# Kernel tuning notes

Measured on AMD Instinct MI355X. Metric: run time of the kernel, lower is better.

The kernel has to match this reference:

```python
import jax, jax.numpy as jnp
import numpy as np

V, E, H = 50000, 128, 256  # vocab, embedding_size, hidden_size
S, B = 512, 64             # seq_len, batch (seq-first, torch LSTM default)


def setup_inputs() -> dict:
    key = jax.random.key(0)
    ks = jax.random.split(key, 10)
    u = 1.0 / np.sqrt(H)  # torch LSTM/Linear init bound

    def unif(k, sh):
        return jax.random.uniform(k, sh, jnp.float32, -u, u)

    emb = jax.random.normal(ks[0], (V, E), jnp.float32) * 0.02
    emb = emb.at[0].set(0.0)  # padding_idx=0

    inp = {
        "seq": jax.random.randint(ks[1], (S, B), 0, V),
        "emb": emb,
        # forward direction weights (gate order i,f,g,o like torch)
        "W_ih_f": unif(ks[2], (4 * H, E)),
        "W_hh_f": unif(ks[3], (4 * H, H)),
        "b_f": unif(ks[4], (4 * H,)),  # b_ih + b_hh fused (identical math)
        # reverse direction
        "W_ih_b": unif(ks[5], (4 * H, E)),
        "W_hh_b": unif(ks[6], (4 * H, H)),
        "b_b": unif(ks[7], (4 * H,)),
        # classification head over concatenated bi-directional features
        "W_out": unif(ks[8], (1, 2 * H)),
        "b_out": unif(ks[9], (1,)),
    }
    return inp


def _lstm_scan(xg, W_hh):
    """xg: [S,B,4H] precomputed input-gate projections; returns hidden seq [S,B,H]."""
    b = xg.shape[1]
    h0 = jnp.zeros((b, H), xg.dtype)
    c0 = jnp.zeros((b, H), xg.dtype)

    def step(carry, xg_t):
        h, c = carry
        gates = xg_t + h @ W_hh.T  # [B,4H]
        i, f, g, o = jnp.split(gates, 4, axis=-1)
        i = jax.nn.sigmoid(i)
        f = jax.nn.sigmoid(f)
        g = jnp.tanh(g)
        o = jax.nn.sigmoid(o)
        c = f * c + i * g
        h = o * jnp.tanh(c)
        return (h, c), h

    _, hs = jax.lax.scan(step, (h0, c0), xg)
    return hs


def reference(seq, emb, W_ih_f, W_hh_f, b_f, W_ih_b, W_hh_b, b_b, W_out, b_out):
    # embedding with padding_idx=0 (row 0 contributes zero)
    x = jnp.where((seq == 0)[..., None], 0.0, emb[seq])  # [S,B,E]

    xg_f = jnp.einsum("sbe,ge->sbg", x, W_ih_f) + b_f          # [S,B,4H]
    hs_f = _lstm_scan(xg_f, W_hh_f)                             # [S,B,H]

    xr = x[::-1]
    xg_b = jnp.einsum("sbe,ge->sbg", xr, W_ih_b) + b_b
    hs_b = _lstm_scan(xg_b, W_hh_b)[::-1]                       # [S,B,H]

    out = jnp.concatenate([hs_f, hs_b], axis=-1)                # [S,B,2H]
    last = out[-1]                                              # [B,2H]
    return jax.nn.sigmoid(last @ W_out.T + b_out)               # [B,1]
```

## Files before the change

### kernel.cpp

```cpp
#include <hip/hip_runtime.h>
#include <hip/hip_bf16.h>
#include <stdint.h>
#include <string.h>

#define S_LEN 512
#define NBATCH 64
#define EDIM 128
#define HDIM 256
#define GDIM 1024

#define WQ_SCALE 1024.0f
#define HQ_SCALE 127.0f
#define LOG2E 1.4426950408889634f
#define C_IFO (-1.1093545e-05f)
#define C_G (2.2187090e-05f)

typedef __attribute__((ext_vector_type(8))) short short8;
typedef __attribute__((ext_vector_type(4))) short short4v;
typedef __attribute__((ext_vector_type(4))) float float4v;
typedef __attribute__((ext_vector_type(4))) int int4v;

#define OFF_WHH8 0u
#define SZ_WHH8 (256u * 64u * 16u)
#define OFF_WIH (OFF_WHH8 + SZ_WHH8)
#define SZ_WIH (64u * 4u * 64u * 16u)
#define OFF_XG ((size_t)(OFF_WIH + SZ_WIH))
#define SZ_XG ((size_t)S_LEN * NBATCH * GDIM * 2)
#define OFF_HF (OFF_XG + SZ_XG)

__device__ __forceinline__ short f2bf(float f) {
    union { float f; unsigned u; } v;
    v.f = f;
    unsigned r = (v.u + 0x7fffu + ((v.u >> 16) & 1u)) >> 16;
    return (short)r;
}
__device__ __forceinline__ float bf2f(short s) {
    union { unsigned u; float f; } v;
    v.u = ((unsigned)(unsigned short)s) << 16;
    return v.f;
}
__device__ __forceinline__ float sigm(float x) {
    float e = __expf(-x);
    return __builtin_amdgcn_rcpf(1.0f + e);
}
__device__ __forceinline__ float tanh_(float x) {
    float e = __expf(2.0f * x);
    return 1.0f - 2.0f * __builtin_amdgcn_rcpf(e + 1.0f);
}

__global__ __launch_bounds__(256) void prep_frags(const float* __restrict__ src,
                                                  char* __restrict__ dst,
                                                  int K, int nchunks, int nfrags) {
    int id = blockIdx.x * blockDim.x + threadIdx.x;
    int lane = id & 63;
    int f = id >> 6;
    if (f >= nfrags) return;
    int tile = f / nchunks;
    int c = f - tile * nchunks;
    int row = tile * 16 + (lane & 15);
    int k0 = c * 32 + ((lane >> 4) * 8);
    const float* s = src + (size_t)row * K + k0;
    short8 pack;
#pragma unroll
    for (int j = 0; j < 8; ++j) pack[j] = f2bf(s[j]);
    *(short8*)(dst + ((size_t)f * 64 + lane) * 16) = pack;
}

__global__ __launch_bounds__(256) void prep_whh_i8(const float* __restrict__ src,
                                                   char* __restrict__ dst) {
    int id = blockIdx.x * blockDim.x + threadIdx.x;
    int lane = id & 63;
    int f = id >> 6;
    int tile = f >> 2, kc = f & 3;
    int row = tile * 16 + (lane & 15);
    int k0 = kc * 64 + ((lane >> 4) * 16);
    const float* s = src + (size_t)row * HDIM + k0;
    union { char b[16]; int4v v; } u;
#pragma unroll
    for (int b = 0; b < 16; ++b)
        u.b[b] = (char)(int)rintf(s[b] * WQ_SCALE);
    *(int4v*)(dst + ((size_t)f * 64 + lane) * 16) = u.v;
}

__global__ __launch_bounds__(256) void input_proj(const int* __restrict__ seq,
                                                  const float* __restrict__ emb,
                                                  const char* __restrict__ wih_frags,
                                                  const float* __restrict__ bias,
                                                  char* __restrict__ xg) {
    __shared__ __align__(16) short lx[4][16][136];
    int tid = threadIdx.x;
    int t0 = blockIdx.x * 4;
    int g = blockIdx.y;

    {
        int row = tid >> 2;
        int tt = row >> 4, m = row & 15;
        int k0 = (tid & 3) * 32;
        int v = seq[(t0 + tt) * NBATCH + g * 16 + m];
        const float* src = emb + (size_t)v * EDIM + k0;
        bool zero = (v == 0);
#pragma unroll
        for (int u = 0; u < 32; u += 4) {
            float4v f = *(const float4v*)(src + u);
            short4v p;
#pragma unroll
            for (int e = 0; e < 4; ++e) p[e] = zero ? (short)0 : f2bf(f[e]);
            *(short4v*)&lx[tt][m][k0 + u] = p;
        }
    }
    __syncthreads();

    int lane = tid & 63, w = tid >> 6;
    int ln = lane & 15, q = lane >> 4;

    short8 Bx[4][4];
#pragma unroll
    for (int tt = 0; tt < 4; ++tt)
#pragma unroll
        for (int c = 0; c < 4; ++c)
            Bx[tt][c] = *(const short8*)&lx[tt][ln][c * 32 + q * 8];

    for (int nt = 0; nt < 16; ++nt) {
        int tile = w * 16 + nt;
        float kg = ((tile >> 4) == 2) ? (2.0f * LOG2E) : (-LOG2E);
        short8 Aw[4];
#pragma unroll
        for (int c = 0; c < 4; ++c)
            Aw[c] = *(const short8*)(wih_frags + (((size_t)tile * 4 + c) * 64 + lane) * 16);
        float4v b4 = *(const float4v*)(bias + tile * 16 + q * 4);
#pragma unroll
        for (int tt = 0; tt < 4; ++tt) {
            float4v acc = b4;
#pragma unroll
            for (int c = 0; c < 4; ++c)
                acc = __builtin_amdgcn_mfma_f32_16x16x32_bf16(Aw[c], Bx[tt][c], acc, 0, 0, 0);
            short4v p;
#pragma unroll
            for (int r = 0; r < 4; ++r) p[r] = f2bf(acc[r] * kg);
            size_t off = ((size_t)(t0 + tt) * NBATCH + g * 16 + ln) * GDIM + tile * 16 + q * 4;
            *(short4v*)(xg + off * 2) = p;
        }
    }
}

#define HPAD 320
__global__ __launch_bounds__(1024, 4) void lstm_scan(const char* __restrict__ whh8,
                                                     const char* __restrict__ xg,
                                                     float* __restrict__ hf_out) {
    __shared__ __align__(16) char hls[2][4][HPAD];
    __shared__ __align__(16) int scr[16][256];
    int tid = threadIdx.x;
    int lane = tid & 63, w = tid >> 6;
    int ln = lane & 15, q = lane >> 4;
    int bg = blockIdx.x;

    int4v Wfr[4][4];
#pragma unroll
    for (int g = 0; g < 4; ++g) {
        int tile = g * 16 + w;
#pragma unroll
        for (int kc = 0; kc < 4; ++kc)
            Wfr[g][kc] = *(const int4v*)(whh8 + (((size_t)(tile * 4 + kc)) * 64 + lane) * 16);
    }

    {
        int* hp = (int*)&hls[0][0][0];
        for (int i = tid; i < (2 * 4 * HPAD) / 4; i += 1024) hp[i] = 0;
    }

    const char* hrd = &hls[0][0][0];
    char* hwr = &hls[1][0][0];
    int hoff_rd = (ln & 3) * HPAD + q * 16;

    int b = ln & 3;
    int rr = ln >> 2;
    int j = w * 16 + q * 4 + rr;
    int hoff_wr = b * HPAD + j;

    int* swr = &scr[w][q * 16 + ln * 4];
    const int* srd = &scr[w][q * 16 + b * 4 + rr];

    float cst = 0.0f;

    const char* xgp = xg + (((size_t)(bg * 4 + b) * GDIM + j) * 2);
    const size_t tstep = (size_t)NBATCH * GDIM * 2;

    unsigned short xq[4];
#pragma unroll
    for (int g = 0; g < 4; ++g)
        xq[g] = *(const unsigned short*)(xgp + g * 512);

    __syncthreads();

    const int4v z4 = {0, 0, 0, 0};
    for (int t = 0; t < S_LEN; ++t) {
        int4v Bh[4];
#pragma unroll
        for (int kc = 0; kc < 4; ++kc)
            Bh[kc] = *(const int4v*)(hrd + hoff_rd + kc * 64);

        float xgf[4];
#pragma unroll
        for (int g = 0; g < 4; ++g) xgf[g] = bf2f((short)xq[g]);
        xgp += tstep;
        if (t != S_LEN - 1) {
#pragma unroll
            for (int g = 0; g < 4; ++g)
                xq[g] = *(const unsigned short*)(xgp + g * 512);
        }

        int4v a[4];
#pragma unroll
        for (int g = 0; g < 4; ++g)
            a[g] = __builtin_amdgcn_mfma_i32_16x16x64_i8(Wfr[g][0], Bh[0], z4, 0, 0, 0);
#pragma unroll
        for (int kc = 1; kc < 4; ++kc)
#pragma unroll
            for (int g = 0; g < 4; ++g)
                a[g] = __builtin_amdgcn_mfma_i32_16x16x64_i8(Wfr[g][kc], Bh[kc], a[g], 0, 0, 0);

        if (ln < 4) {
#pragma unroll
            for (int g = 0; g < 4; ++g)
                *(int4v*)(swr + g * 64) = a[g];
        }
        float s0 = fmaf((float)srd[0], C_IFO, xgf[0]);
        float s1 = fmaf((float)srd[64], C_IFO, xgf[1]);
        float s2 = fmaf((float)srd[128], C_G, xgf[2]);
        float s3 = fmaf((float)srd[192], C_IFO, xgf[3]);

        float iv = __builtin_amdgcn_rcpf(1.0f + exp2f(s0));
        float fv = __builtin_amdgcn_rcpf(1.0f + exp2f(s1));
        float gv = fmaf(-2.0f, __builtin_amdgcn_rcpf(1.0f + exp2f(s2)), 1.0f);
        float ov = __builtin_amdgcn_rcpf(1.0f + exp2f(s3));
        float cv = fmaf(fv, cst, iv * gv);
        cst = cv;
        float tc = fmaf(-2.0f, __builtin_amdgcn_rcpf(1.0f + exp2f(cv * (2.0f * LOG2E))), 1.0f);
        float hv = ov * tc;

        int hq = (int)rintf(hv * HQ_SCALE);
        hwr[hoff_wr] = (char)hq;

        if (t == S_LEN - 1)
            hf_out[((size_t)(bg * 4 + b)) * HDIM + j] = hv;

        const char* tr = hrd; hrd = hwr; hwr = (char*)tr;
        __syncthreads();
    }
}

__global__ __launch_bounds__(256) void tail_kernel(const int* __restrict__ seq,
                                                   const float* __restrict__ emb,
                                                   const float* __restrict__ wih_b,
                                                   const float* __restrict__ b_b,
                                                   const float* __restrict__ wout,
                                                   const float* __restrict__ b_out,
                                                   const float* __restrict__ hf,
                                                   float* __restrict__ out) {
    __shared__ float xs[EDIM];
    __shared__ float red[4];
    int b = blockIdx.x, tid = threadIdx.x;
    if (tid < EDIM) {
        int v = seq[(S_LEN - 1) * NBATCH + b];
        xs[tid] = (v == 0) ? 0.0f : emb[(size_t)v * EDIM + tid];
    }
    __syncthreads();

    int j = tid;
    float si = b_b[j], sg = b_b[2 * HDIM + j], so = b_b[3 * HDIM + j];
    const float* wi = wih_b + (size_t)j * EDIM;
    const float* wg = wih_b + (size_t)(2 * HDIM + j) * EDIM;
    const float* wo = wih_b + (size_t)(3 * HDIM + j) * EDIM;
#pragma unroll 8
    for (int k = 0; k < EDIM; k += 4) {
        float4v x4 = *(const float4v*)&xs[k];
        float4v a = *(const float4v*)(wi + k);
        float4v c = *(const float4v*)(wg + k);
        float4v d = *(const float4v*)(wo + k);
#pragma unroll
        for (int e = 0; e < 4; ++e) {
            si += a[e] * x4[e];
            sg += c[e] * x4[e];
            so += d[e] * x4[e];
        }
    }
    float cc = sigm(si) * tanh_(sg);
    float hb = sigm(so) * tanh_(cc);
    float partial = hf[(size_t)b * HDIM + j] * wout[j] + hb * wout[HDIM + j];

    float val = partial;
#pragma unroll
    for (int off = 32; off > 0; off >>= 1) val += __shfl_down(val, off, 64);
    int lane = tid & 63, wv = tid >> 6;
    if (lane == 0) red[wv] = val;
    __syncthreads();
    if (tid == 0) out[b] = sigm(red[0] + red[1] + red[2] + red[3] + b_out[0]);
}

extern "C" void kernel_launch(void* const* d_in, const int* in_sizes, int n_in,
                              void* d_out, int out_size, void* d_ws, size_t ws_size,
                              hipStream_t stream) {
    const int* seq = (const int*)d_in[0];
    const float* emb = (const float*)d_in[1];
    const float* Wih_f = (const float*)d_in[2];
    const float* Whh_f = (const float*)d_in[3];
    const float* b_f = (const float*)d_in[4];
    const float* Wih_b = (const float*)d_in[5];
    const float* b_b = (const float*)d_in[7];
    const float* Wout = (const float*)d_in[8];
    const float* b_out = (const float*)d_in[9];
    float* out = (float*)d_out;
    char* ws = (char*)d_ws;

    prep_whh_i8<<<dim3(64), 256, 0, stream>>>(Whh_f, ws + OFF_WHH8);
    prep_frags<<<dim3(64), 256, 0, stream>>>(Wih_f, ws + OFF_WIH, EDIM, 4, 64 * 4);
    input_proj<<<dim3(S_LEN / 4, 4), 256, 0, stream>>>(seq, emb, ws + OFF_WIH, b_f, ws + OFF_XG);
    lstm_scan<<<dim3(16), 1024, 0, stream>>>(ws + OFF_WHH8, ws + OFF_XG, (float*)(ws + OFF_HF));
    tail_kernel<<<dim3(NBATCH), 256, 0, stream>>>(seq, emb, Wih_b, b_b, Wout, b_out,
                                                  (const float*)(ws + OFF_HF), out);
}
```

Baseline: 704.1 us.

## Fuse input projection and LSTM scan into one kernel with flag-based chunk handoff

Merges the two weight-prep kernels into one setup kernel and fuses input projection with the recurrent scan in a single launch. Producer blocks compute 4-timestep chunks of gate inputs and bump per-chunk flags, while 16 scan blocks spin on those flags, so the recurrence can start before the whole projection finishes. This removes launch gaps and the serial dependency between projection and scan. It relies on producer blocks being scheduled before or alongside the spinning scan blocks; block-index ordering makes that likely, though it is not guaranteed. The per-step flag polling and acquire loads also add cost inside the serial loop.

```diff
diff --git a/kernel.cpp b/kernel.cpp
--- a/kernel.cpp
+++ b/kernel.cpp
@@ -27,6 +27,7 @@
 #define OFF_XG ((size_t)(OFF_WIH + SZ_WIH))
 #define SZ_XG ((size_t)S_LEN * NBATCH * GDIM * 2)
 #define OFF_HF (OFF_XG + SZ_XG)
+#define OFF_FLAGS (OFF_HF + (size_t)NBATCH * HDIM * 4)
 
 __device__ __forceinline__ short f2bf(float f) {
     union { float f; unsigned u; } v;
@@ -48,204 +49,228 @@
     return 1.0f - 2.0f * __builtin_amdgcn_rcpf(e + 1.0f);
 }
 
-__global__ __launch_bounds__(256) void prep_frags(const float* __restrict__ src,
-                                                  char* __restrict__ dst,
-                                                  int K, int nchunks, int nfrags) {
-    int id = blockIdx.x * blockDim.x + threadIdx.x;
-    int lane = id & 63;
-    int f = id >> 6;
-    if (f >= nfrags) return;
-    int tile = f / nchunks;
-    int c = f - tile * nchunks;
-    int row = tile * 16 + (lane & 15);
-    int k0 = c * 32 + ((lane >> 4) * 8);
-    const float* s = src + (size_t)row * K + k0;
-    short8 pack;
-#pragma unroll
-    for (int j = 0; j < 8; ++j) pack[j] = f2bf(s[j]);
-    *(short8*)(dst + ((size_t)f * 64 + lane) * 16) = pack;
-}
-
-__global__ __launch_bounds__(256) void prep_whh_i8(const float* __restrict__ src,
-                                                   char* __restrict__ dst) {
-    int id = blockIdx.x * blockDim.x + threadIdx.x;
-    int lane = id & 63;
-    int f = id >> 6;
-    int tile = f >> 2, kc = f & 3;
-    int row = tile * 16 + (lane & 15);
-    int k0 = kc * 64 + ((lane >> 4) * 16);
-    const float* s = src + (size_t)row * HDIM + k0;
-    union { char b[16]; int4v v; } u;
-#pragma unroll
-    for (int b = 0; b < 16; ++b)
-        u.b[b] = (char)(int)rintf(s[b] * WQ_SCALE);
-    *(int4v*)(dst + ((size_t)f * 64 + lane) * 16) = u.v;
-}
-
-__global__ __launch_bounds__(256) void input_proj(const int* __restrict__ seq,
-                                                  const float* __restrict__ emb,
-                                                  const char* __restrict__ wih_frags,
-                                                  const float* __restrict__ bias,
-                                                  char* __restrict__ xg) {
-    __shared__ __align__(16) short lx[4][16][136];
+__global__ __launch_bounds__(256) void setup_kernel(const float* __restrict__ whh_src,
+                                                    const float* __restrict__ wih_src,
+                                                    char* __restrict__ whh_dst,
+                                                    char* __restrict__ wih_dst,
+                                                    int* __restrict__ flags) {
+    int bx = blockIdx.x;
     int tid = threadIdx.x;
-    int t0 = blockIdx.x * 4;
-    int g = blockIdx.y;
-
-    {
-        int row = tid >> 2;
-        int tt = row >> 4, m = row & 15;
-        int k0 = (tid & 3) * 32;
-        int v = seq[(t0 + tt) * NBATCH + g * 16 + m];
-        const float* src = emb + (size_t)v * EDIM + k0;
-        bool zero = (v == 0);
-#pragma unroll
-        for (int u = 0; u < 32; u += 4) {
-            float4v f = *(const float4v*)(src + u);
-            short4v p;
-#pragma unroll
-            for (int e = 0; e < 4; ++e) p[e] = zero ? (short)0 : f2bf(f[e]);
-            *(short4v*)&lx[tt][m][k0 + u] = p;
-        }
+    if (bx < 64) {
+        int id = bx * 256 + tid;
+        int lane = id & 63;
+        int f = id >> 6;
+        int tile = f >> 2, kc = f & 3;
+        int row = tile * 16 + (lane & 15);
+        int k0 = kc * 64 + ((lane >> 4) * 16);
+        const float* s = whh_src + (size_t)row * HDIM + k0;
+        union { char b[16]; int4v v; } u;
+#pragma unroll
+        for (int b = 0; b < 16; ++b)
+            u.b[b] = (char)(int)rintf(s[b] * WQ_SCALE);
+        *(int4v*)(whh_dst + ((size_t)f * 64 + lane) * 16) = u.v;
+    } else if (bx < 128) {
+        int id = (bx - 64) * 256 + tid;
+        int lane = id & 63;
+        int f = id >> 6;
+        int tile = f >> 2;
+        int c = f & 3;
+        int row = tile * 16 + (lane & 15);
+        int k0 = c * 32 + ((lane >> 4) * 8);
+        const float* s = wih_src + (size_t)row * EDIM + k0;
+        short8 pack;
+#pragma unroll
+        for (int j = 0; j < 8; ++j) pack[j] = f2bf(s[j]);
+        *(short8*)(wih_dst + ((size_t)f * 64 + lane) * 16) = pack;
+    } else {
+        if (tid < 128) flags[tid] = 0;
     }
-    __syncthreads();
-
-    int lane = tid & 63, w = tid >> 6;
-    int ln = lane & 15, q = lane >> 4;
-
-    short8 Bx[4][4];
-#pragma unroll
-    for (int tt = 0; tt < 4; ++tt)
-#pragma unroll
-        for (int c = 0; c < 4; ++c)
-            Bx[tt][c] = *(const short8*)&lx[tt][ln][c * 32 + q * 8];
-
-    for (int nt = 0; nt < 16; ++nt) {
-        int tile = w * 16 + nt;
-        float kg = ((tile >> 4) == 2) ? (2.0f * LOG2E) : (-LOG2E);
-        short8 Aw[4];
-#pragma unroll
-        for (int c = 0; c < 4; ++c)
-            Aw[c] = *(const short8*)(wih_frags + (((size_t)tile * 4 + c) * 64 + lane) * 16);
-        float4v b4 = *(const float4v*)(bias + tile * 16 + q * 4);
-#pragma unroll
-        for (int tt = 0; tt < 4; ++tt) {
-            float4v acc = b4;
+}
+
+#define HPAD 320
+__global__ __launch_bounds__(1024, 4) void mega_kernel(const int* __restrict__ seq,
+                                                       const float* __restrict__ emb,
+                                                       const char* __restrict__ wih_frags,
+                                                       const float* __restrict__ bias_f,
+                                                       char* __restrict__ xg,
+                                                       const char* __restrict__ whh8,
+                                                       float* __restrict__ hf_out,
+                                                       int* __restrict__ flags) {
+    if (blockIdx.x < 512) {
+        __shared__ __align__(16) short lx[4][16][136];
+        int tid = threadIdx.x;
+        int p = blockIdx.x;
+        int t0 = (p >> 2) * 4;
+        int g16 = p & 3;
+
+        {
+            int row = tid >> 4;
+            int tt = row >> 4, m = row & 15;
+            int k0 = (tid & 15) * 8;
+            int v = seq[(t0 + tt) * NBATCH + g16 * 16 + m];
+            const float* src = emb + (size_t)v * EDIM + k0;
+            bool zero = (v == 0);
+#pragma unroll
+            for (int u = 0; u < 8; u += 4) {
+                float4v f = *(const float4v*)(src + u);
+                short4v pk;
+#pragma unroll
+                for (int e = 0; e < 4; ++e) pk[e] = zero ? (short)0 : f2bf(f[e]);
+                *(short4v*)&lx[tt][m][k0 + u] = pk;
+            }
+        }
+        __syncthreads();
+
+        int lane = tid & 63, w = tid >> 6;
+        int ln = lane & 15, q = lane >> 4;
+
+        short8 Bx[4][4];
+#pragma unroll
+        for (int tt = 0; tt < 4; ++tt)
 #pragma unroll
             for (int c = 0; c < 4; ++c)
-                acc = __builtin_amdgcn_mfma_f32_16x16x32_bf16(Aw[c], Bx[tt][c], acc, 0, 0, 0);
-            short4v p;
-#pragma unroll
-            for (int r = 0; r < 4; ++r) p[r] = f2bf(acc[r] * kg);
-            size_t off = ((size_t)(t0 + tt) * NBATCH + g * 16 + ln) * GDIM + tile * 16 + q * 4;
-            *(short4v*)(xg + off * 2) = p;
-        }
-    }
-}
-
-#define HPAD 320
-__global__ __launch_bounds__(1024, 4) void lstm_scan(const char* __restrict__ whh8,
-                                                     const char* __restrict__ xg,
-                                                     float* __restrict__ hf_out) {
-    __shared__ __align__(16) char hls[2][4][HPAD];
-    __shared__ __align__(16) int scr[16][256];
-    int tid = threadIdx.x;
-    int lane = tid & 63, w = tid >> 6;
-    int ln = lane & 15, q = lane >> 4;
-    int bg = blockIdx.x;
-
-    int4v Wfr[4][4];
-#pragma unroll
-    for (int g = 0; g < 4; ++g) {
-        int tile = g * 16 + w;
-#pragma unroll
-        for (int kc = 0; kc < 4; ++kc)
-            Wfr[g][kc] = *(const int4v*)(whh8 + (((size_t)(tile * 4 + kc)) * 64 + lane) * 16);
-    }
-
-    {
-        int* hp = (int*)&hls[0][0][0];
-        for (int i = tid; i < (2 * 4 * HPAD) / 4; i += 1024) hp[i] = 0;
-    }
-
-    const char* hrd = &hls[0][0][0];
-    char* hwr = &hls[1][0][0];
-    int hoff_rd = (ln & 3) * HPAD + q * 16;
-
-    int b = ln & 3;
-    int rr = ln >> 2;
-    int j = w * 16 + q * 4 + rr;
-    int hoff_wr = b * HPAD + j;
-
-    int* swr = &scr[w][q * 16 + ln * 4];
-    const int* srd = &scr[w][q * 16 + b * 4 + rr];
-
-    float cst = 0.0f;
-
-    const char* xgp = xg + (((size_t)(bg * 4 + b) * GDIM + j) * 2);
-    const size_t tstep = (size_t)NBATCH * GDIM * 2;
-
-    unsigned short xq[4];
-#pragma unroll
-    for (int g = 0; g < 4; ++g)
-        xq[g] = *(const unsigned short*)(xgp + g * 512);
-
-    __syncthreads();
-
-    const int4v z4 = {0, 0, 0, 0};
-    for (int t = 0; t < S_LEN; ++t) {
-        int4v Bh[4];
-#pragma unroll
-        for (int kc = 0; kc < 4; ++kc)
-            Bh[kc] = *(const int4v*)(hrd + hoff_rd + kc * 64);
-
-        float xgf[4];
-#pragma unroll
-        for (int g = 0; g < 4; ++g) xgf[g] = bf2f((short)xq[g]);
-        xgp += tstep;
-        if (t != S_LEN - 1) {
+                Bx[tt][c] = *(const short8*)&lx[tt][ln][c * 32 + q * 8];
+
+#pragma unroll
+        for (int nt = 0; nt < 4; ++nt) {
+            int tile = w * 4 + nt;
+            float kg = ((tile >> 4) == 2) ? (2.0f * LOG2E) : (-LOG2E);
+            short8 Aw[4];
+#pragma unroll
+            for (int c = 0; c < 4; ++c)
+                Aw[c] = *(const short8*)(wih_frags + (((size_t)tile * 4 + c) * 64 + lane) * 16);
+            float4v b4 = *(const float4v*)(bias_f + tile * 16 + q * 4);
+#pragma unroll
+            for (int tt = 0; tt < 4; ++tt) {
+                float4v acc = b4;
+#pragma unroll
+                for (int c = 0; c < 4; ++c)
+                    acc = __builtin_amdgcn_mfma_f32_16x16x32_bf16(Aw[c], Bx[tt][c], acc, 0, 0, 0);
+                short4v pk;
+#pragma unroll
+                for (int r = 0; r < 4; ++r) pk[r] = f2bf(acc[r] * kg);
+                size_t off = ((size_t)(t0 + tt) * NBATCH + g16 * 16 + ln) * GDIM + tile * 16 + q * 4;
+                *(short4v*)(xg + off * 2) = pk;
+            }
+        }
+        __syncthreads();
+        if (tid == 0)
+            __hip_atomic_fetch_add(&flags[p >> 2], 1, __ATOMIC_RELEASE,
+                                   __HIP_MEMORY_SCOPE_AGENT);
+    } else {
+        __shared__ __align__(16) char hls[2][4][HPAD];
+        __shared__ __align__(16) int scr[16][256];
+        int tid = threadIdx.x;
+        int lane = tid & 63, w = tid >> 6;
+        int ln = lane & 15, q = lane >> 4;
+        int bg = blockIdx.x - 512;
+
+        int4v Wfr[4][4];
+#pragma unroll
+        for (int g = 0; g < 4; ++g) {
+            int tile = g * 16 + w;
+#pragma unroll
+            for (int kc = 0; kc < 4; ++kc)
+                Wfr[g][kc] = *(const int4v*)(whh8 + (((size_t)(tile * 4 + kc)) * 64 + lane) * 16);
+        }
+
+        {
+            int* hp = (int*)&hls[0][0][0];
+            for (int i = tid; i < (2 * 4 * HPAD) / 4; i += 1024) hp[i] = 0;
+        }
+
+        const char* hrd = &hls[0][0][0];
+        char* hwr = &hls[1][0][0];
+        int hoff_rd = (ln & 3) * HPAD + q * 16;
+
+        int b = ln & 3;
+        int rr = ln >> 2;
+        int j = w * 16 + q * 4 + rr;
+        int hoff_wr = b * HPAD + j;
+
+        int* swr = &scr[w][q * 16 + ln * 4];
+        const int* srd = &scr[w][q * 16 + b * 4 + rr];
+
+        float cst = 0.0f;
+
+        const char* xgp = xg + (((size_t)(bg * 4 + b) * GDIM + j) * 2);
+        const size_t tstep = (size_t)NBATCH * GDIM * 2;
+
+        int ready_upto = 0;
+#define WAIT_CHUNK(ch)                                                          \
+        while (ready_upto <= (ch)) {                                            \
+            int fv = __hip_atomic_load(&flags[ready_upto], __ATOMIC_ACQUIRE,    \
+                                       __HIP_MEMORY_SCOPE_AGENT);               \
+            if (fv >= 4) ++ready_upto;                                          \
+            else __builtin_amdgcn_s_sleep(2);                                   \
+        }
+
+        WAIT_CHUNK(0);
+        unsigned short xq[4];
+#pragma unroll
+        for (int g = 0; g < 4; ++g)
+            xq[g] = *(const unsigned short*)(xgp + g * 512);
+
+        __syncthreads();
+
+        const int4v z4 = {0, 0, 0, 0};
+        for (int t = 0; t < S_LEN; ++t) {
+            int4v Bh[4];
+#pragma unroll
+            for (int kc = 0; kc < 4; ++kc)
+                Bh[kc] = *(const int4v*)(hrd + hoff_rd + kc * 64);
+
+            float xgf[4];
+#pragma unroll
+            for (int g = 0; g < 4; ++g) xgf[g] = bf2f((short)xq[g]);
+            xgp += tstep;
+            if (t != S_LEN - 1) {
+                int ch = (t + 1) >> 2;
+                WAIT_CHUNK(ch);
+#pragma unroll
+                for (int g = 0; g < 4; ++g)
+                    xq[g] = *(const unsigned short*)(xgp + g * 512);
+            }
+
+            int4v a[4];
 #pragma unroll
             for (int g = 0; g < 4; ++g)
-                xq[g] = *(const unsigned short*)(xgp + g * 512);
-        }
-
-        int4v a[4];
-#pragma unroll
-        for (int g = 0; g < 4; ++g)
-            a[g] = __builtin_amdgcn_mfma_i32_16x16x64_i8(Wfr[g][0], Bh[0], z4, 0, 0, 0);
-#pragma unroll
-        for (int kc = 1; kc < 4; ++kc)
-#pragma unroll
-            for (int g = 0; g < 4; ++g)
-                a[g] = __builtin_amdgcn_mfma_i32_16x16x64_i8(Wfr[g][kc], Bh[kc], a[g], 0, 0, 0);
-
-        if (ln < 4) {
-#pragma unroll
-            for (int g = 0; g < 4; ++g)
-                *(int4v*)(swr + g * 64) = a[g];
-        }
-        float s0 = fmaf((float)srd[0], C_IFO, xgf[0]);
-        float s1 = fmaf((float)srd[64], C_IFO, xgf[1]);
-        float s2 = fmaf((float)srd[128], C_G, xgf[2]);
-        float s3 = fmaf((float)srd[192], C_IFO, xgf[3]);
-
-        float iv = __builtin_amdgcn_rcpf(1.0f + exp2f(s0));
-        float fv = __builtin_amdgcn_rcpf(1.0f + exp2f(s1));
-        float gv = fmaf(-2.0f, __builtin_amdgcn_rcpf(1.0f + exp2f(s2)), 1.0f);
-        float ov = __builtin_amdgcn_rcpf(1.0f + exp2f(s3));
-        float cv = fmaf(fv, cst, iv * gv);
-        cst = cv;
-        float tc = fmaf(-2.0f, __builtin_amdgcn_rcpf(1.0f + exp2f(cv * (2.0f * LOG2E))), 1.0f);
-        float hv = ov * tc;
-
-        int hq = (int)rintf(hv * HQ_SCALE);
-        hwr[hoff_wr] = (char)hq;
-
-        if (t == S_LEN - 1)
-            hf_out[((size_t)(bg * 4 + b)) * HDIM + j] = hv;
-
-        const char* tr = hrd; hrd = hwr; hwr = (char*)tr;
-        __syncthreads();
+                a[g] = __builtin_amdgcn_mfma_i32_16x16x64_i8(Wfr[g][0], Bh[0], z4, 0, 0, 0);
+#pragma unroll
+            for (int kc = 1; kc < 4; ++kc)
+#pragma unroll
+                for (int g = 0; g < 4; ++g)
+                    a[g] = __builtin_amdgcn_mfma_i32_16x16x64_i8(Wfr[g][kc], Bh[kc], a[g], 0, 0, 0);
+
+            if (ln < 4) {
+#pragma unroll
+                for (int g = 0; g < 4; ++g)
+                    *(int4v*)(swr + g * 64) = a[g];
+            }
+            float s0 = fmaf((float)srd[0], C_IFO, xgf[0]);
+            float s1 = fmaf((float)srd[64], C_IFO, xgf[1]);
+            float s2 = fmaf((float)srd[128], C_G, xgf[2]);
+            float s3 = fmaf((float)srd[192], C_IFO, xgf[3]);
+
+            float iv = __builtin_amdgcn_rcpf(1.0f + exp2f(s0));
+            float fv = __builtin_amdgcn_rcpf(1.0f + exp2f(s1));
+            float gv = fmaf(-2.0f, __builtin_amdgcn_rcpf(1.0f + exp2f(s2)), 1.0f);
+            float ov = __builtin_amdgcn_rcpf(1.0f + exp2f(s3));
+            float cv = fmaf(fv, cst, iv * gv);
+            cst = cv;
+            float tc = fmaf(-2.0f, __builtin_amdgcn_rcpf(1.0f + exp2f(cv * (2.0f * LOG2E))), 1.0f);
+            float hv = ov * tc;
+
+            int hq = (int)rintf(hv * HQ_SCALE);
+            hwr[hoff_wr] = (char)hq;
+
+            if (t == S_LEN - 1)
+                hf_out[((size_t)(bg * 4 + b)) * HDIM + j] = hv;
+
+            const char* tr = hrd; hrd = hwr; hwr = (char*)tr;
+            __syncthreads();
+        }
+#undef WAIT_CHUNK
     }
 }
 
@@ -311,11 +336,13 @@
     const float* b_out = (const float*)d_in[9];
     float* out = (float*)d_out;
     char* ws = (char*)d_ws;
-
-    prep_whh_i8<<<dim3(64), 256, 0, stream>>>(Whh_f, ws + OFF_WHH8);
-    prep_frags<<<dim3(64), 256, 0, stream>>>(Wih_f, ws + OFF_WIH, EDIM, 4, 64 * 4);
-    input_proj<<<dim3(S_LEN / 4, 4), 256, 0, stream>>>(seq, emb, ws + OFF_WIH, b_f, ws + OFF_XG);
-    lstm_scan<<<dim3(16), 1024, 0, stream>>>(ws + OFF_WHH8, ws + OFF_XG, (float*)(ws + OFF_HF));
+    int* flags = (int*)(ws + OFF_FLAGS);
+
+    setup_kernel<<<dim3(129), 256, 0, stream>>>(Whh_f, Wih_f, ws + OFF_WHH8,
+                                                ws + OFF_WIH, flags);
+    mega_kernel<<<dim3(528), 1024, 0, stream>>>(seq, emb, ws + OFF_WIH, b_f,
+                                                ws + OFF_XG, ws + OFF_WHH8,
+                                                (float*)(ws + OFF_HF), flags);
     tail_kernel<<<dim3(NBATCH), 256, 0, stream>>>(seq, emb, Wih_b, b_b, Wout, b_out,
                                                   (const float*)(ws + OFF_HF), out);
 }
```

Measured after the change: 804.8 us. 1.14x slower.
